# Kernel optimization log

Hardware: AMD Instinct MI355X
Metric: run time of the kernel (lower is better)

The kernel has to match this reference:

```python
import jax, jax.numpy as jnp
import numpy as np

B, S, D = 4, 4096, 128

def setup_inputs() -> dict:
    key = jax.random.key(0)
    ks = jax.random.split(key, 7)
    s = 1.0 / np.sqrt(D)
    return {
        "x": jax.random.normal(ks[0], (B, S, D), dtype=jnp.float32),
        "Wq": jax.random.normal(ks[1], (D, D), dtype=jnp.float32) * s,
        "bq": jax.random.normal(ks[2], (D,), dtype=jnp.float32) * s,
        "Wk": jax.random.normal(ks[3], (D, D), dtype=jnp.float32) * s,
        "bk": jax.random.normal(ks[4], (D,), dtype=jnp.float32) * s,
        "Wv": jax.random.normal(ks[5], (D, D), dtype=jnp.float32) * s,
        "bv": jax.random.normal(ks[6], (D,), dtype=jnp.float32) * s,
    }

def reference(x, Wq, bq, Wk, bk, Wv, bv):
    # Linear projections (torch Linear: x @ W^T + b)
    Q = jnp.einsum('bsd,ed->bse', x, Wq) + bq
    K = jnp.einsum('bsd,ed->bse', x, Wk) + bk
    V = jnp.einsum('bsd,ed->bse', x, Wv) + bv
    scale = jnp.sqrt(jnp.asarray(x.shape[-1], dtype=x.dtype))
    scores = jnp.einsum('bqd,bkd->bqk', Q, K) / scale  # [B,S,S]
    weights = jax.nn.softmax(scores, axis=-1)
    return jnp.einsum('bqk,bkd->bqd', weights, V)
```

## Files before the change

kernel.cpp:

```cpp
#include <hip/hip_runtime.h>
#include <hip/hip_bf16.h>
#include <stdint.h>

#define NB 4
#define NS 4096
#define ND 128
#define KVBLK 32
#define NT32 (NS / KVBLK)
#define QBLK 128

typedef __attribute__((ext_vector_type(8))) short short8;
typedef __attribute__((ext_vector_type(4))) float f32x4;
typedef __attribute__((ext_vector_type(16))) float f32x16;
typedef __attribute__((ext_vector_type(2))) int i32x2;
typedef _Float16 f16;

#define QSCALE 0.12751744f

__device__ __forceinline__ unsigned short f2bfu(float f) {
  __hip_bfloat16 h = __float2bfloat16(f);
  union { __hip_bfloat16 h; unsigned short u; } c; c.h = h; return c.u;
}
__device__ __forceinline__ uint32_t pack2bf(float lo, float hi) {
  return (uint32_t)f2bfu(lo) | ((uint32_t)f2bfu(hi) << 16);
}

__device__ __forceinline__ void gl_lds16(const void* g, void* l) {
  __builtin_amdgcn_global_load_lds(
      (const __attribute__((address_space(1))) uint32_t*)g,
      (__attribute__((address_space(3))) uint32_t*)l, 16, 0, 0);
}

#define MFMA16(a, b, c) __builtin_amdgcn_mfma_f32_16x16x32_bf16((a), (b), (c), 0, 0, 0)
#define MFMA32(a, b, c) __builtin_amdgcn_mfma_f32_32x32x16_bf16((a), (b), (c), 0, 0, 0)

#if __has_builtin(__builtin_amdgcn_permlane32_swap)
#define PLSWAP(lo_, hi_)                                                        \
  { i32x2 r_ = __builtin_amdgcn_permlane32_swap((int)(lo_), (int)(hi_), false,  \
                                                false);                         \
    lo_ = (uint32_t)r_[0]; hi_ = (uint32_t)r_[1]; }
#else
#define PLSWAP(lo_, hi_)                                                        \
  { uint32_t sA_ = hi ? (lo_) : (hi_);                                          \
    uint32_t rA_ = (uint32_t)__shfl_xor((int)sA_, 32, 64);                      \
    uint32_t nl_ = hi ? rA_ : (lo_);                                            \
    uint32_t nh_ = hi ? (hi_) : rA_;                                            \
    lo_ = nl_; hi_ = nh_; }
#endif

__global__ __launch_bounds__(512) void preconv_kernel(
    const float* __restrict__ x,
    const float* __restrict__ Wq, const float* __restrict__ Wk,
    const float* __restrict__ Wv,
    unsigned short* __restrict__ xb, unsigned short* __restrict__ Wb)
{
  const size_t xg8 = (size_t)NB * NS * ND / 8;
  size_t i = (size_t)blockIdx.x * 512 + threadIdx.x;
  const float* src; unsigned short* dst; size_t off;
  if (i < xg8) { src = x; dst = xb; off = i * 8; }
  else {
    size_t j = i - xg8;
    int which = (int)(j / 2048);
    src = which == 0 ? Wq : which == 1 ? Wk : Wv;
    dst = Wb;
    off = j * 8;
    src = src - (size_t)which * 16384;
  }
  float4 a = *(const float4*)(src + off), b2 = *(const float4*)(src + off + 4);
  short8 o;
  o[0] = (short)f2bfu(a.x);  o[1] = (short)f2bfu(a.y);
  o[2] = (short)f2bfu(a.z);  o[3] = (short)f2bfu(a.w);
  o[4] = (short)f2bfu(b2.x); o[5] = (short)f2bfu(b2.y);
  o[6] = (short)f2bfu(b2.z); o[7] = (short)f2bfu(b2.w);
  *(short8*)(dst + off) = o;
}

__global__ __launch_bounds__(256) void proj_kernel(
    const unsigned short* __restrict__ xb, const unsigned short* __restrict__ Wb,
    const float* __restrict__ bq, const float* __restrict__ bk,
    const float* __restrict__ bv,
    unsigned short* __restrict__ Qo, unsigned short* __restrict__ Ko,
    unsigned short* __restrict__ Vt)
{
  __shared__ unsigned short Xs[64 * 128];
  __shared__ unsigned short Ws[128 * 128];

  const int tile = blockIdx.x, b = blockIdx.y, which = blockIdx.z;
  const float* bias = which == 0 ? bq : which == 1 ? bk : bv;
  const int t = threadIdx.x, wave = t >> 6, lane = t & 63;
  const int lr = lane & 15, lg = lane >> 4;

  const char* xsrc = (const char*)(xb + ((size_t)b * NS + (size_t)tile * 64) * ND);
#pragma unroll
  for (int i = wave; i < 16; i += 4) {
    int y = i * 1024 + lane * 16;
    int so = y ^ (((y >> 8) & 7) << 4);
    gl_lds16(xsrc + so, (char*)Xs + y);
  }
  const char* wsrc = (const char*)(Wb + (size_t)which * 16384);
#pragma unroll
  for (int i = wave; i < 32; i += 4) {
    int y = i * 1024 + lane * 16;
    int so = y ^ (((y >> 8) & 7) << 4);
    gl_lds16(wsrc + so, (char*)Ws + y);
  }
  __syncthreads();

  short8 af[4];
#pragma unroll
  for (int kk = 0; kk < 4; ++kk) {
    int row = wave * 16 + lr;
    int ba = (row * 256 + kk * 64 + lg * 16) ^ ((row & 7) << 4);
    af[kk] = *(const short8*)((const char*)Xs + ba);
  }
  f32x4 acc[8] = {};
#pragma unroll
  for (int kk = 0; kk < 4; ++kk) {
#pragma unroll
    for (int nf = 0; nf < 8; ++nf) {
      int n = nf * 16 + lr;
      int ba = (n * 256 + kk * 64 + lg * 16) ^ ((n & 7) << 4);
      short8 bf = *(const short8*)((const char*)Ws + ba);
      acc[nf] = MFMA16(af[kk], bf, acc[nf]);
    }
  }

  if (which < 2) {
    unsigned short* Out = (which == 0) ? Qo : Ko;
    const float sc = (which == 0) ? QSCALE : 1.0f;
#pragma unroll
    for (int nf = 0; nf < 8; ++nf) {
      float bb = bias[nf * 16 + lr];
#pragma unroll
      for (int r = 0; r < 4; ++r) {
        float v = (acc[nf][r] + bb) * sc;
        int row = tile * 64 + wave * 16 + lg * 4 + r;
        Out[((size_t)b * NS + row) * ND + nf * 16 + lr] = f2bfu(v);
      }
    }
  } else {
    __syncthreads();
    unsigned short* Tt = Ws;
#pragma unroll
    for (int nf = 0; nf < 8; ++nf) {
      float bb = bias[nf * 16 + lr];
#pragma unroll
      for (int r = 0; r < 4; ++r) {
        int e = nf * 16 + lr;
        int sl = wave * 16 + lg * 4 + r;
        Tt[e * 72 + sl] = f2bfu(acc[nf][r] + bb);
      }
    }
    __syncthreads();
    int e = t >> 1, off = (t & 1) * 32;
    const short8* src = (const short8*)(Tt + e * 72 + off);
    short8* dst = (short8*)(Vt + ((size_t)b * ND + e) * NS + (size_t)tile * 64 + off);
#pragma unroll
    for (int i = 0; i < 4; ++i) dst[i] = src[i];
  }
}

__global__ __launch_bounds__(256, 3) void attn_kernel(
    const unsigned short* __restrict__ Q, const unsigned short* __restrict__ K,
    const unsigned short* __restrict__ Vt, f16* __restrict__ OP,
    float* __restrict__ Mp, float* __restrict__ Lp, int nchunk)
{
  __shared__ char smem[32768];

  const int Lid = blockIdx.x;
  const int ngroups = NB * nchunk;
  int g, qt;
  if ((ngroups & 7) == 0) {
    int xcd = Lid & 7, s2 = Lid >> 3;
    qt = s2 & 31;
    g = xcd * (ngroups >> 3) + (s2 >> 5);
  } else { qt = Lid & 31; g = Lid >> 5; }
  const int b = g / nchunk, c = g - b * nchunk;

  const int cbase = NT32 / nchunk, crem = NT32 - cbase * nchunk;
  const int tstart = c * cbase + (c < crem ? c : crem);
  const int ntpc = cbase + (c < crem ? 1 : 0);

  const int t = threadIdx.x, wave = t >> 6, lane = t & 63;
  const int lq = lane & 31, hi = lane >> 5;

  const int qrow = qt * QBLK + wave * 32 + lq;
  short8 qf[8];
  const unsigned short* Qb = Q + ((size_t)b * NS + qrow) * ND;
#pragma unroll
  for (int kt = 0; kt < 8; ++kt) qf[kt] = *(const short8*)(Qb + kt * 16 + hi * 8);

  const char* Kbase = (const char*)(K + (size_t)b * NS * ND) +
                      (size_t)tstart * (KVBLK * ND * 2);
  const char* Vbase = (const char*)(Vt + (size_t)b * ND * NS) +
                      (size_t)tstart * (KVBLK * 2);

  short8 rk[2], rv[2];
  auto ldKV = [&](int tt) {
    const char* ksrc = Kbase + (size_t)tt * 8192;
    const char* vsrc = Vbase + (size_t)tt * 64;
#pragma unroll
    for (int j = 0; j < 2; ++j) {
      int y = (wave * 2 + j) * 1024 + lane * 16;
      int so = y ^ (((y >> 8) & 7) << 4);
      rk[j] = *(const short8*)(ksrc + so);
      int d = y >> 6, col = y & 63;
      int cx = col ^ (((d >> 1) & 3) << 4);
      rv[j] = *(const short8*)(vsrc + (size_t)d * (NS * 2) + cx);
    }
  };
  auto wrKV = [&](int p) {
    char* kd = smem + p * 8192;
    char* vd = smem + 16384 + p * 8192;
#pragma unroll
    for (int j = 0; j < 2; ++j) {
      int y = (wave * 2 + j) * 1024 + lane * 16;
      *(short8*)(kd + y) = rk[j];
      *(short8*)(vd + y) = rv[j];
    }
  };

  f32x16 oacc[4] = {};
  float m = -1e30f, l = 0.f;

  ldKV(0);
  wrKV(0);
  __syncthreads();

  for (int tt = 0; tt < ntpc; ++tt) {
    const int p = tt & 1;
    const char* kb = smem + p * 8192;
    const char* vb = smem + 16384 + p * 8192;
    const bool more = (tt + 1 < ntpc);
    if (more) ldKV(tt + 1);

    f32x16 s0 = {};
    __builtin_amdgcn_s_setprio(1);
#pragma unroll
    for (int kt = 0; kt < 8; ++kt) {
      int co = (kt * 32 + hi * 16) ^ ((lq & 7) << 4);
      short8 k0 = *(const short8*)(kb + lq * 256 + co);
      s0 = MFMA32(k0, qf[kt], s0);
    }
    __builtin_amdgcn_s_setprio(0);

    float x0 = fmaxf(s0[0], s0[1]), x1 = fmaxf(s0[2], s0[3]);
    float x2 = fmaxf(s0[4], s0[5]), x3 = fmaxf(s0[6], s0[7]);
#pragma unroll
    for (int r = 8; r < 16; r += 4) {
      x0 = fmaxf(x0, s0[r]);     x1 = fmaxf(x1, s0[r + 1]);
      x2 = fmaxf(x2, s0[r + 2]); x3 = fmaxf(x3, s0[r + 3]);
    }
    float px = fmaxf(fmaxf(x0, x1), fmaxf(x2, x3));
    px = fmaxf(px, __shfl_xor(px, 32, 64));
    if (__any(px > m + 8.f)) {
      float mn = fmaxf(m, px);
      float corr = exp2f(m - mn);
      m = mn;
      l *= corr;
#pragma unroll
      for (int dt = 0; dt < 4; ++dt)
#pragma unroll
        for (int r = 0; r < 16; ++r) oacc[dt][r] *= corr;
    }

    float p0[16];
    float u0 = 0.f, u1 = 0.f, u2 = 0.f, u3 = 0.f;
#pragma unroll
    for (int r = 0; r < 16; r += 4) {
      p0[r]     = exp2f(s0[r] - m);
      p0[r + 1] = exp2f(s0[r + 1] - m);
      p0[r + 2] = exp2f(s0[r + 2] - m);
      p0[r + 3] = exp2f(s0[r + 3] - m);
      u0 += p0[r]; u1 += p0[r + 1]; u2 += p0[r + 2]; u3 += p0[r + 3];
    }
    l += (u0 + u1) + (u2 + u3);

    uint32_t pk[8];
#pragma unroll
    for (int i = 0; i < 8; ++i) pk[i] = pack2bf(p0[2 * i], p0[2 * i + 1]);
    short8 pfrag[2];
#pragma unroll
    for (int kt2 = 0; kt2 < 2; ++kt2) {
      uint32_t e0 = pk[4 * kt2 + 0], e1 = pk[4 * kt2 + 1];
      uint32_t e2 = pk[4 * kt2 + 2], e3 = pk[4 * kt2 + 3];
      PLSWAP(e0, e2);
      PLSWAP(e1, e3);
      union { uint32_t u[4]; short8 s; } pf;
      pf.u[0] = e0; pf.u[1] = e1; pf.u[2] = e2; pf.u[3] = e3;
      pfrag[kt2] = pf.s;
    }

    const int vsw = ((lq >> 1) & 3) << 4;
    __builtin_amdgcn_s_setprio(1);
#pragma unroll
    for (int dt = 0; dt < 4; ++dt) {
      int rowb = (dt * 32 + lq) * 64;
#pragma unroll
      for (int kt2 = 0; kt2 < 2; ++kt2) {
        int co = (kt2 * 32 + hi * 16) ^ vsw;
        short8 vf = *(const short8*)(vb + rowb + co);
        oacc[dt] = MFMA32(vf, pfrag[kt2], oacc[dt]);
      }
    }
    __builtin_amdgcn_s_setprio(0);

    if (more) wrKV(p ^ 1);
    __syncthreads();
  }

  float lt = l + __shfl_xor(l, 32, 64);
  f16* OPb = OP + ((size_t)(c * NB + b) * ND) * NS + qrow;
#pragma unroll
  for (int dt = 0; dt < 4; ++dt)
#pragma unroll
    for (int r = 0; r < 16; ++r) {
      int d = dt * 32 + (r & 3) + 8 * (r >> 2) + 4 * hi;
      OPb[(size_t)d * NS] = (f16)oacc[dt][r];
    }
  if (hi == 0) {
    Mp[(size_t)(c * NB + b) * NS + qrow] = m;
    Lp[(size_t)(c * NB + b) * NS + qrow] = lt;
  }
}

template <int NC>
__global__ __launch_bounds__(256) void combine_kernel(
    const f16* __restrict__ OP, const float* __restrict__ Mp,
    const float* __restrict__ Lp, float* __restrict__ Out)
{
  __shared__ float wn[NC][64];
  __shared__ float LT[64][129];

  const int qtile = blockIdx.x, b = blockIdx.y;
  const int t = threadIdx.x;

  if (t < 64) {
    size_t qg = (size_t)qtile * 64 + t;
    float mv[NC], wloc[NC];
#pragma unroll
    for (int cc = 0; cc < NC; ++cc)
      mv[cc] = Mp[(size_t)(cc * NB + b) * NS + qg];
    float mx = mv[0];
#pragma unroll
    for (int cc = 1; cc < NC; ++cc) mx = fmaxf(mx, mv[cc]);
    float Lt = 0.f;
#pragma unroll
    for (int cc = 0; cc < NC; ++cc) {
      float w = exp2f(mv[cc] - mx);
      Lt += w * Lp[(size_t)(cc * NB + b) * NS + qg];
      wloc[cc] = w;
    }
    float inv = 1.0f / Lt;
#pragma unroll
    for (int cc = 0; cc < NC; ++cc) wn[cc][t] = wloc[cc] * inv;
  }
  __syncthreads();

  const int so = (t & 7) * 8;
  const int dl = t >> 3;
  const size_t sbase = (size_t)qtile * 64 + so;
#pragma unroll
  for (int dblk = 0; dblk < 4; ++dblk) {
    int d = dblk * 32 + dl;
    float a0 = 0, a1 = 0, a2 = 0, a3 = 0, a4 = 0, a5 = 0, a6 = 0, a7 = 0;
#pragma unroll
    for (int cc = 0; cc < NC; ++cc) {
      const f16* src = OP + ((size_t)(cc * NB + b) * ND + d) * NS + sbase;
      short8 v = *(const short8*)src;
      const float* w = &wn[cc][so];
      union { short s; f16 h; } u;
      u.s = v[0]; a0 += w[0] * (float)u.h;
      u.s = v[1]; a1 += w[1] * (float)u.h;
      u.s = v[2]; a2 += w[2] * (float)u.h;
      u.s = v[3]; a3 += w[3] * (float)u.h;
      u.s = v[4]; a4 += w[4] * (float)u.h;
      u.s = v[5]; a5 += w[5] * (float)u.h;
      u.s = v[6]; a6 += w[6] * (float)u.h;
      u.s = v[7]; a7 += w[7] * (float)u.h;
    }
    LT[so + 0][d] = a0; LT[so + 1][d] = a1;
    LT[so + 2][d] = a2; LT[so + 3][d] = a3;
    LT[so + 4][d] = a4; LT[so + 5][d] = a5;
    LT[so + 6][d] = a6; LT[so + 7][d] = a7;
  }
  __syncthreads();

  const int d2 = t & 127, qh = t >> 7;
  float* Ob = Out + ((size_t)b * NS + (size_t)qtile * 64) * ND;
#pragma unroll 8
  for (int pass = 0; pass < 32; ++pass) {
    int qq = pass * 2 + qh;
    Ob[(size_t)qq * ND + d2] = LT[qq][d2];
  }
}

extern "C" void kernel_launch(void* const* d_in, const int* in_sizes, int n_in,
                              void* d_out, int out_size, void* d_ws, size_t ws_size,
                              hipStream_t stream) {
  const float* x  = (const float*)d_in[0];
  const float* Wq = (const float*)d_in[1];
  const float* bq = (const float*)d_in[2];
  const float* Wk = (const float*)d_in[3];
  const float* bk = (const float*)d_in[4];
  const float* Wv = (const float*)d_in[5];
  const float* bv = (const float*)d_in[6];

  const size_t elems = (size_t)NB * NS * ND;
  char* base = (char*)d_ws;
  unsigned short* Qw  = (unsigned short*)base;
  unsigned short* Kw  = Qw + elems;
  unsigned short* Vtw = Kw + elems;
  char* region2 = base + 3 * elems * 2;

  int nchunk = 6;
  for (;;) {
    size_t need = 3 * elems * 2 +
                  (size_t)nchunk * (elems * 2 + 2 * (size_t)NB * NS * 4);
    if (need <= ws_size || nchunk == 1) break;
    nchunk = (nchunk == 6) ? 4 : nchunk >> 1;
  }

  unsigned short* xb16 = (unsigned short*)region2;
  unsigned short* Wb16 = xb16 + elems;
  f16* OPw = (f16*)region2;
  float* Mpw = (float*)(region2 + (size_t)nchunk * elems * 2);
  float* Lpw = Mpw + (size_t)nchunk * NB * NS;

  preconv_kernel<<<dim3(524), 512, 0, stream>>>(x, Wq, Wk, Wv, xb16, Wb16);

  proj_kernel<<<dim3(NS / 64, NB, 3), 256, 0, stream>>>(
      xb16, Wb16, bq, bk, bv, Qw, Kw, Vtw);

  attn_kernel<<<dim3(32 * NB * nchunk), 256, 0, stream>>>(
      Qw, Kw, Vtw, OPw, Mpw, Lpw, nchunk);

  dim3 cgrid(NS / 64, NB);
  switch (nchunk) {
    case 6: combine_kernel<6><<<cgrid, 256, 0, stream>>>(OPw, Mpw, Lpw, (float*)d_out); break;
    case 4: combine_kernel<4><<<cgrid, 256, 0, stream>>>(OPw, Mpw, Lpw, (float*)d_out); break;
    case 2: combine_kernel<2><<<cgrid, 256, 0, stream>>>(OPw, Mpw, Lpw, (float*)d_out); break;
    default: combine_kernel<1><<<cgrid, 256, 0, stream>>>(OPw, Mpw, Lpw, (float*)d_out); break;
  }
}
```

Before: 76.73 us.

## Fuse split-KV combine into attention kernel via last-block atomic counter

Removes the separate combine kernel launch. The last attention block to finish for each (batch, q-tile) does the reduction, found through an atomic counter plus threadfences. The number of KV chunks becomes a template parameter, with a default of 8 instead of 6. Occupancy is raised to 4 waves via launch bounds, and the K/V shared-memory write is moved ahead of the PV MFMA loop for better overlap. In exchange the code needs a memset per launch, adds register pressure, and puts the combine work on only 128 tail blocks.

```diff
diff --git a/kernel.cpp b/kernel.cpp
--- a/kernel.cpp
+++ b/kernel.cpp
@@ -160,26 +160,27 @@
   }
 }
 
-__global__ __launch_bounds__(256, 3) void attn_kernel(
+template <int NC>
+__global__ __launch_bounds__(256, 4) void attn_kernel(
     const unsigned short* __restrict__ Q, const unsigned short* __restrict__ K,
     const unsigned short* __restrict__ Vt, f16* __restrict__ OP,
-    float* __restrict__ Mp, float* __restrict__ Lp, int nchunk)
+    float* __restrict__ Mp, float* __restrict__ Lp,
+    float* __restrict__ Out, int* __restrict__ cnt)
 {
-  __shared__ char smem[32768];
+  __shared__ char smem[38912];
 
   const int Lid = blockIdx.x;
-  const int ngroups = NB * nchunk;
+  constexpr int ngroups = NB * NC;
   int g, qt;
-  if ((ngroups & 7) == 0) {
+  if constexpr ((ngroups & 7) == 0) {
     int xcd = Lid & 7, s2 = Lid >> 3;
     qt = s2 & 31;
     g = xcd * (ngroups >> 3) + (s2 >> 5);
   } else { qt = Lid & 31; g = Lid >> 5; }
-  const int b = g / nchunk, c = g - b * nchunk;
-
-  const int cbase = NT32 / nchunk, crem = NT32 - cbase * nchunk;
-  const int tstart = c * cbase + (c < crem ? c : crem);
-  const int ntpc = cbase + (c < crem ? 1 : 0);
+  const int b = g / NC, c = g - b * NC;
+
+  constexpr int ntpc = NT32 / NC;
+  const int tstart = c * ntpc;
 
   const int t = threadIdx.x, wave = t >> 6, lane = t & 63;
   const int lq = lane & 31, hi = lane >> 5;
@@ -291,6 +292,8 @@
       pfrag[kt2] = pf.s;
     }
 
+    if (more) wrKV(p ^ 1);
+
     const int vsw = ((lq >> 1) & 3) << 4;
     __builtin_amdgcn_s_setprio(1);
 #pragma unroll
@@ -305,7 +308,6 @@
     }
     __builtin_amdgcn_s_setprio(0);
 
-    if (more) wrKV(p ^ 1);
     __syncthreads();
   }
 
@@ -322,21 +324,22 @@
     Mp[(size_t)(c * NB + b) * NS + qrow] = m;
     Lp[(size_t)(c * NB + b) * NS + qrow] = lt;
   }
-}
-
-template <int NC>
-__global__ __launch_bounds__(256) void combine_kernel(
-    const f16* __restrict__ OP, const float* __restrict__ Mp,
-    const float* __restrict__ Lp, float* __restrict__ Out)
-{
-  __shared__ float wn[NC][64];
-  __shared__ float LT[64][129];
-
-  const int qtile = blockIdx.x, b = blockIdx.y;
-  const int t = threadIdx.x;
-
-  if (t < 64) {
-    size_t qg = (size_t)qtile * 64 + t;
+
+  __threadfence();
+  __syncthreads();
+  int* flagp = (int*)(smem + 38904);
+  if (t == 0) {
+    int old = atomicAdd(&cnt[b * 32 + qt], 1);
+    *flagp = (old == NC - 1);
+  }
+  __syncthreads();
+  if (!*flagp) return;
+  __threadfence();
+
+  float* wn = (float*)smem;
+  float* LTb = (float*)(smem + 4096);
+  if (t < 128) {
+    size_t qg = (size_t)qt * 128 + t;
     float mv[NC], wloc[NC];
 #pragma unroll
     for (int cc = 0; cc < NC; ++cc)
@@ -353,45 +356,48 @@
     }
     float inv = 1.0f / Lt;
 #pragma unroll
-    for (int cc = 0; cc < NC; ++cc) wn[cc][t] = wloc[cc] * inv;
+    for (int cc = 0; cc < NC; ++cc) wn[cc * 128 + t] = wloc[cc] * inv;
   }
   __syncthreads();
 
-  const int so = (t & 7) * 8;
-  const int dl = t >> 3;
-  const size_t sbase = (size_t)qtile * 64 + so;
-#pragma unroll
-  for (int dblk = 0; dblk < 4; ++dblk) {
-    int d = dblk * 32 + dl;
-    float a0 = 0, a1 = 0, a2 = 0, a3 = 0, a4 = 0, a5 = 0, a6 = 0, a7 = 0;
-#pragma unroll
-    for (int cc = 0; cc < NC; ++cc) {
-      const f16* src = OP + ((size_t)(cc * NB + b) * ND + d) * NS + sbase;
-      short8 v = *(const short8*)src;
-      const float* w = &wn[cc][so];
-      union { short s; f16 h; } u;
-      u.s = v[0]; a0 += w[0] * (float)u.h;
-      u.s = v[1]; a1 += w[1] * (float)u.h;
-      u.s = v[2]; a2 += w[2] * (float)u.h;
-      u.s = v[3]; a3 += w[3] * (float)u.h;
-      u.s = v[4]; a4 += w[4] * (float)u.h;
-      u.s = v[5]; a5 += w[5] * (float)u.h;
-      u.s = v[6]; a6 += w[6] * (float)u.h;
-      u.s = v[7]; a7 += w[7] * (float)u.h;
-    }
-    LT[so + 0][d] = a0; LT[so + 1][d] = a1;
-    LT[so + 2][d] = a2; LT[so + 3][d] = a3;
-    LT[so + 4][d] = a4; LT[so + 5][d] = a5;
-    LT[so + 6][d] = a6; LT[so + 7][d] = a7;
-  }
-  __syncthreads();
-
-  const int d2 = t & 127, qh = t >> 7;
-  float* Ob = Out + ((size_t)b * NS + (size_t)qtile * 64) * ND;
+#pragma unroll
+  for (int half = 0; half < 2; ++half) {
+    const int so = (t & 7) * 8;
+    const int dl = t >> 3;
+    const size_t sbase = (size_t)qt * 128 + half * 64 + so;
+#pragma unroll
+    for (int dblk = 0; dblk < 4; ++dblk) {
+      int d = dblk * 32 + dl;
+      float a0 = 0, a1 = 0, a2 = 0, a3 = 0, a4 = 0, a5 = 0, a6 = 0, a7 = 0;
+#pragma unroll
+      for (int cc = 0; cc < NC; ++cc) {
+        const f16* src = OP + ((size_t)(cc * NB + b) * ND + d) * NS + sbase;
+        short8 v = *(const short8*)src;
+        const float* w = wn + cc * 128 + half * 64 + so;
+        union { short s; f16 h; } u;
+        u.s = v[0]; a0 += w[0] * (float)u.h;
+        u.s = v[1]; a1 += w[1] * (float)u.h;
+        u.s = v[2]; a2 += w[2] * (float)u.h;
+        u.s = v[3]; a3 += w[3] * (float)u.h;
+        u.s = v[4]; a4 += w[4] * (float)u.h;
+        u.s = v[5]; a5 += w[5] * (float)u.h;
+        u.s = v[6]; a6 += w[6] * (float)u.h;
+        u.s = v[7]; a7 += w[7] * (float)u.h;
+      }
+      LTb[(so + 0) * 129 + d] = a0; LTb[(so + 1) * 129 + d] = a1;
+      LTb[(so + 2) * 129 + d] = a2; LTb[(so + 3) * 129 + d] = a3;
+      LTb[(so + 4) * 129 + d] = a4; LTb[(so + 5) * 129 + d] = a5;
+      LTb[(so + 6) * 129 + d] = a6; LTb[(so + 7) * 129 + d] = a7;
+    }
+    __syncthreads();
+    const int d2 = t & 127, qh = t >> 7;
+    float* Ob = Out + ((size_t)b * NS + (size_t)qt * 128 + half * 64) * ND;
 #pragma unroll 8
-  for (int pass = 0; pass < 32; ++pass) {
-    int qq = pass * 2 + qh;
-    Ob[(size_t)qq * ND + d2] = LT[qq][d2];
+    for (int pass = 0; pass < 32; ++pass) {
+      int qq = pass * 2 + qh;
+      Ob[(size_t)qq * ND + d2] = LTb[qq * 129 + d2];
+    }
+    __syncthreads();
   }
 }
 
@@ -413,12 +419,12 @@
   unsigned short* Vtw = Kw + elems;
   char* region2 = base + 3 * elems * 2;
 
-  int nchunk = 6;
-  for (;;) {
+  int nchunk = 8;
+  while (nchunk > 1) {
     size_t need = 3 * elems * 2 +
-                  (size_t)nchunk * (elems * 2 + 2 * (size_t)NB * NS * 4);
-    if (need <= ws_size || nchunk == 1) break;
-    nchunk = (nchunk == 6) ? 4 : nchunk >> 1;
+                  (size_t)nchunk * (elems * 2 + 2 * (size_t)NB * NS * 4) + 1024;
+    if (need <= ws_size) break;
+    nchunk >>= 1;
   }
 
   unsigned short* xb16 = (unsigned short*)region2;
@@ -426,20 +432,24 @@
   f16* OPw = (f16*)region2;
   float* Mpw = (float*)(region2 + (size_t)nchunk * elems * 2);
   float* Lpw = Mpw + (size_t)nchunk * NB * NS;
+  int* cntw = (int*)(Lpw + (size_t)nchunk * NB * NS);
+
+  hipMemsetAsync(cntw, 0, NB * 32 * sizeof(int), stream);
 
   preconv_kernel<<<dim3(524), 512, 0, stream>>>(x, Wq, Wk, Wv, xb16, Wb16);
 
   proj_kernel<<<dim3(NS / 64, NB, 3), 256, 0, stream>>>(
       xb16, Wb16, bq, bk, bv, Qw, Kw, Vtw);
 
-  attn_kernel<<<dim3(32 * NB * nchunk), 256, 0, stream>>>(
-      Qw, Kw, Vtw, OPw, Mpw, Lpw, nchunk);
-
-  dim3 cgrid(NS / 64, NB);
+  float* out = (float*)d_out;
   switch (nchunk) {
-    case 6: combine_kernel<6><<<cgrid, 256, 0, stream>>>(OPw, Mpw, Lpw, (float*)d_out); break;
-    case 4: combine_kernel<4><<<cgrid, 256, 0, stream>>>(OPw, Mpw, Lpw, (float*)d_out); break;
-    case 2: combine_kernel<2><<<cgrid, 256, 0, stream>>>(OPw, Mpw, Lpw, (float*)d_out); break;
-    default: combine_kernel<1><<<cgrid, 256, 0, stream>>>(OPw, Mpw, Lpw, (float*)d_out); break;
-  }
-}
+    case 8: attn_kernel<8><<<dim3(32 * NB * 8), 256, 0, stream>>>(
+                Qw, Kw, Vtw, OPw, Mpw, Lpw, out, cntw); break;
+    case 4: attn_kernel<4><<<dim3(32 * NB * 4), 256, 0, stream>>>(
+                Qw, Kw, Vtw, OPw, Mpw, Lpw, out, cntw); break;
+    case 2: attn_kernel<2><<<dim3(32 * NB * 2), 256, 0, stream>>>(
+                Qw, Kw, Vtw, OPw, Mpw, Lpw, out, cntw); break;
+    default: attn_kernel<1><<<dim3(32 * NB * 1), 256, 0, stream>>>(
+                Qw, Kw, Vtw, OPw, Mpw, Lpw, out, cntw); break;
+  }
+}
```

After: 303.8 us. 296% more time.

## Stage K/V tiles directly from global to LDS, widen K swizzle

Applied to the files above, without the earlier changes.

Replaces the register-staged prefetch of the next K/V tile (global load into registers, then LDS write after compute) with direct global-to-LDS loads issued at the start of each iteration. This frees the prefetch registers and removes the separate LDS store phase. The K swizzle widens from 8 to 16 rows so it matches the new layout and reduces bank conflicts. The softmax probabilities are also computed in place in the score registers. The change relies on gl_lds16 being defined elsewhere, and on async LDS loads finishing by the barrier.

```diff
diff --git a/kernel.cpp b/kernel.cpp
--- a/kernel.cpp
+++ b/kernel.cpp
@@ -195,50 +195,40 @@
   const char* Vbase = (const char*)(Vt + (size_t)b * ND * NS) +
                       (size_t)tstart * (KVBLK * 2);
 
-  short8 rk[2], rv[2];
-  auto ldKV = [&](int tt) {
+  auto stage = [&](int p, int tt) {
     const char* ksrc = Kbase + (size_t)tt * 8192;
     const char* vsrc = Vbase + (size_t)tt * 64;
+    char* kd = smem + p * 8192;
+    char* vd = smem + 16384 + p * 8192;
 #pragma unroll
     for (int j = 0; j < 2; ++j) {
       int y = (wave * 2 + j) * 1024 + lane * 16;
-      int so = y ^ (((y >> 8) & 7) << 4);
-      rk[j] = *(const short8*)(ksrc + so);
+      int so = y ^ (((y >> 8) & 15) << 4);
+      gl_lds16(ksrc + so, kd + y);
       int d = y >> 6, col = y & 63;
       int cx = col ^ (((d >> 1) & 3) << 4);
-      rv[j] = *(const short8*)(vsrc + (size_t)d * (NS * 2) + cx);
-    }
-  };
-  auto wrKV = [&](int p) {
-    char* kd = smem + p * 8192;
-    char* vd = smem + 16384 + p * 8192;
-#pragma unroll
-    for (int j = 0; j < 2; ++j) {
-      int y = (wave * 2 + j) * 1024 + lane * 16;
-      *(short8*)(kd + y) = rk[j];
-      *(short8*)(vd + y) = rv[j];
+      gl_lds16(vsrc + (size_t)d * (NS * 2) + cx, vd + y);
     }
   };
 
   f32x16 oacc[4] = {};
   float m = -1e30f, l = 0.f;
 
-  ldKV(0);
-  wrKV(0);
+  stage(0, 0);
   __syncthreads();
 
   for (int tt = 0; tt < ntpc; ++tt) {
     const int p = tt & 1;
     const char* kb = smem + p * 8192;
     const char* vb = smem + 16384 + p * 8192;
-    const bool more = (tt + 1 < ntpc);
-    if (more) ldKV(tt + 1);
+    if (tt + 1 < ntpc) stage(p ^ 1, tt + 1);
 
     f32x16 s0 = {};
+    const int ksw = (lq & 15) << 4;
     __builtin_amdgcn_s_setprio(1);
 #pragma unroll
     for (int kt = 0; kt < 8; ++kt) {
-      int co = (kt * 32 + hi * 16) ^ ((lq & 7) << 4);
+      int co = (kt * 32 + hi * 16) ^ ksw;
       short8 k0 = *(const short8*)(kb + lq * 256 + co);
       s0 = MFMA32(k0, qf[kt], s0);
     }
@@ -264,21 +254,20 @@
         for (int r = 0; r < 16; ++r) oacc[dt][r] *= corr;
     }
 
-    float p0[16];
     float u0 = 0.f, u1 = 0.f, u2 = 0.f, u3 = 0.f;
 #pragma unroll
     for (int r = 0; r < 16; r += 4) {
-      p0[r]     = exp2f(s0[r] - m);
-      p0[r + 1] = exp2f(s0[r + 1] - m);
-      p0[r + 2] = exp2f(s0[r + 2] - m);
-      p0[r + 3] = exp2f(s0[r + 3] - m);
-      u0 += p0[r]; u1 += p0[r + 1]; u2 += p0[r + 2]; u3 += p0[r + 3];
+      s0[r]     = exp2f(s0[r] - m);
+      s0[r + 1] = exp2f(s0[r + 1] - m);
+      s0[r + 2] = exp2f(s0[r + 2] - m);
+      s0[r + 3] = exp2f(s0[r + 3] - m);
+      u0 += s0[r]; u1 += s0[r + 1]; u2 += s0[r + 2]; u3 += s0[r + 3];
     }
     l += (u0 + u1) + (u2 + u3);
 
     uint32_t pk[8];
 #pragma unroll
-    for (int i = 0; i < 8; ++i) pk[i] = pack2bf(p0[2 * i], p0[2 * i + 1]);
+    for (int i = 0; i < 8; ++i) pk[i] = pack2bf(s0[2 * i], s0[2 * i + 1]);
     short8 pfrag[2];
 #pragma unroll
     for (int kt2 = 0; kt2 < 2; ++kt2) {
@@ -305,7 +294,6 @@
     }
     __builtin_amdgcn_s_setprio(0);
 
-    if (more) wrKV(p ^ 1);
     __syncthreads();
   }
 
```

Measured after the change: 75.08 us. 1.02x faster.
